# Kernel optimization log

Hardware: AMD Instinct MI355X
Metric: run time of the kernel (lower is better)

The kernel has to match this reference:

```python
import jax, jax.numpy as jnp
import numpy as np

B, S, H, V, NL = 64, 2048, 512, 50257, 2

def setup_inputs() -> dict:
    key = jax.random.key(0)
    ks = jax.random.split(key, 20)
    s = 0.02
    return {
        "input_ids": jax.random.randint(ks[0], (B,), 0, V),
        "hidden": jax.random.normal(ks[1], (NL, B, H), jnp.float32),
        "block_attn_weights": jax.random.uniform(ks[2], (B, 32), jnp.float32),
        "encoder_outputs": jax.random.normal(ks[3], (B, S, H), jnp.float32),
        "n_blocks": 32,
        "emb": jax.random.normal(ks[4], (V, H), jnp.float32) * s,
        "attn_W": jax.random.normal(ks[5], (H, H), jnp.float32) * s,
        "attn_b": jnp.zeros((H,), jnp.float32),
        "W_ih0": jax.random.normal(ks[6], (3 * H, 2 * H), jnp.float32) * s,
        "W_hh0": jax.random.normal(ks[7], (3 * H, H), jnp.float32) * s,
        "b_ih0": jnp.zeros((3 * H,), jnp.float32),
        "b_hh0": jnp.zeros((3 * H,), jnp.float32),
        "W_ih1": jax.random.normal(ks[8], (3 * H, H), jnp.float32) * s,
        "W_hh1": jax.random.normal(ks[9], (3 * H, H), jnp.float32) * s,
        "b_ih1": jnp.zeros((3 * H,), jnp.float32),
        "b_hh1": jnp.zeros((3 * H,), jnp.float32),
        "out_W": jax.random.normal(ks[10], (V, 2 * H), jnp.float32) * s,
        "out_b": jnp.zeros((V,), jnp.float32),
    }

def _gru_cell(x, h, W_ih, W_hh, b_ih, b_hh):
    gx = x @ W_ih.T + b_ih            # [B, 3H]
    gh = h @ W_hh.T + b_hh            # [B, 3H]
    xr, xz, xn = jnp.split(gx, 3, axis=-1)
    hr, hz, hn = jnp.split(gh, 3, axis=-1)
    r = jax.nn.sigmoid(xr + hr)
    z = jax.nn.sigmoid(xz + hz)
    n = jnp.tanh(xn + r * hn)
    return (1.0 - z) * n + z * h

def reference(input_ids, hidden, block_attn_weights, encoder_outputs, n_blocks,
              emb, attn_W, attn_b, W_ih0, W_hh0, b_ih0, b_hh0,
              W_ih1, W_hh1, b_ih1, b_hh1, out_W, out_b):
    b, s, h = encoder_outputs.shape
    L = s // n_blocks
    eo = encoder_outputs.reshape(b, n_blocks, L, h)          # [B,N,L,H]
    # Luong general score: h_dec . (W e + b), per block
    energy = jnp.einsum('bnlh,gh->bnlg', eo, attn_W) + attn_b  # [B,N,L,H]
    scores = jnp.einsum('bh,bnlh->bnl', hidden[-1], energy)    # [B,N,L]
    attn_w = jax.nn.softmax(scores, axis=-1)                   # [B,N,L]
    block_ctx = jnp.einsum('bnl,bnlh->bnh', attn_w, eo)        # [B,N,H]
    context = jnp.einsum('bn,bnh->bh', block_attn_weights, block_ctx)  # [B,H]
    embedded = emb[input_ids]                                  # [B,H]
    x = jnp.concatenate([embedded, context], axis=-1)          # [B,2H]
    h0 = _gru_cell(x, hidden[0], W_ih0, W_hh0, b_ih0, b_hh0)
    h1 = _gru_cell(h0, hidden[1], W_ih1, W_hh1, b_ih1, b_hh1)
    new_hidden = jnp.stack([h0, h1], axis=0)                   # [NL,B,H]
    out_in = jnp.concatenate([h1, context], axis=-1)           # [B,2H]
    log_probs = jax.nn.log_softmax(out_in @ out_W.T + out_b, axis=-1)  # [B,V]
    return (log_probs, new_hidden, context, attn_w)
```

## Files before the change

### kernel.cpp

```cpp
#include <hip/hip_runtime.h>

#define B_  64
#define S_  2048
#define H_  512
#define V_  50257
#define NB_ 32
#define L_  64
#define H3_ 1536
#define NBLK_OUT 786

typedef float  f32x4  __attribute__((ext_vector_type(4)));
typedef __bf16 bf16x8 __attribute__((ext_vector_type(8)));

struct alignas(16) U4 { unsigned int x, y, z, w; };

__device__ __forceinline__ unsigned int f2bf_bits(float f) {
  unsigned int u = __float_as_uint(f);
  return (u + 0x7fffu + ((u >> 16) & 1u)) >> 16;
}

__device__ __forceinline__ f32x4 ntload4(const float* p) {
  return __builtin_nontemporal_load((const f32x4*)p);
}

__device__ __forceinline__ bf16x8 cvt8(f32x4 w0, f32x4 w1) {
  bf16x8 r;
  r[0] = (__bf16)w0.x; r[1] = (__bf16)w0.y; r[2] = (__bf16)w0.z; r[3] = (__bf16)w0.w;
  r[4] = (__bf16)w1.x; r[5] = (__bf16)w1.y; r[6] = (__bf16)w1.z; r[7] = (__bf16)w1.w;
  return r;
}

__device__ __forceinline__ float wave_sum(float v) {
#pragma unroll
  for (int off = 32; off > 0; off >>= 1) v += __shfl_xor(v, off, 64);
  return v;
}

__global__ __launch_bounds__(128) void k_q(const float* __restrict__ hidden,
                                           const float* __restrict__ attn_W,
                                           float* __restrict__ q) {
  __shared__ float sh[2 * H_];
  int tid = threadIdx.x;
  int h  = blockIdx.x * 128 + tid;
  int b0 = blockIdx.y * 2;
  const float* h1 = hidden + B_ * H_;
  for (int i = tid; i < 2 * H_; i += 128) sh[i] = h1[b0 * H_ + i];
  __syncthreads();
  float acc0 = 0.f, acc1 = 0.f;
  for (int g = 0; g < H_; ++g) {
    float w = attn_W[(size_t)g * H_ + h];
    acc0 += sh[g] * w;
    acc1 += sh[H_ + g] * w;
  }
  q[(b0 + 0) * H_ + h] = acc0;
  q[(b0 + 1) * H_ + h] = acc1;
}

__global__ __launch_bounds__(512) void k_attn(
    const float* __restrict__ eo, const float* __restrict__ hidden,
    const float* __restrict__ attn_b, const float* __restrict__ q,
    float* __restrict__ bc, float* __restrict__ attnw_out) {
  __shared__ float sm[8], ss[8];
  __shared__ float shA[8][H_];
  int tid = threadIdx.x;
  int wv = tid >> 6, lane = tid & 63;
  int idx = blockIdx.x;
  int b = idx >> 5, n = idx & 31;

  f32x4 q0 = *(const f32x4*)(q + (size_t)b * H_ + lane * 4);
  f32x4 q1 = *(const f32x4*)(q + (size_t)b * H_ + 256 + lane * 4);

  const float* hp = hidden + (size_t)B_ * H_ + (size_t)b * H_;
  f32x4 hx = *(const f32x4*)(hp + lane * 4);
  f32x4 hy = *(const f32x4*)(hp + 256 + lane * 4);
  f32x4 ax = *(const f32x4*)(attn_b + lane * 4);
  f32x4 ay = *(const f32x4*)(attn_b + 256 + lane * 4);
  float c0 = hx.x*ax.x + hx.y*ax.y + hx.z*ax.z + hx.w*ax.w
           + hy.x*ay.x + hy.y*ay.y + hy.z*ay.z + hy.w*ay.w;
  c0 = wave_sum(c0);

  const float* eb = eo + (size_t)(b * NB_ + n) * L_ * H_ + (size_t)(wv * 8) * H_;
  float m = -1e30f, s = 0.f;
  float sall[8];
  f32x4 A0 = {0,0,0,0}, A1 = {0,0,0,0};
#pragma unroll
  for (int half = 0; half < 2; ++half) {
    const float* rb = eb + (size_t)(half * 4) * H_;
    f32x4 r0[4], r1[4];
#pragma unroll
    for (int i = 0; i < 4; ++i) {
      r0[i] = ntload4(rb + (size_t)i * H_ + lane * 4);
      r1[i] = ntload4(rb + (size_t)i * H_ + 256 + lane * 4);
    }
    float sc[4];
#pragma unroll
    for (int i = 0; i < 4; ++i)
      sc[i] = r0[i].x*q0.x + r0[i].y*q0.y + r0[i].z*q0.z + r0[i].w*q0.w
            + r1[i].x*q1.x + r1[i].y*q1.y + r1[i].z*q1.z + r1[i].w*q1.w;
#pragma unroll
    for (int off = 32; off > 0; off >>= 1) {
#pragma unroll
      for (int i = 0; i < 4; ++i) sc[i] += __shfl_xor(sc[i], off, 64);
    }
    float w[4];
#pragma unroll
    for (int i = 0; i < 4; ++i) { sc[i] += c0; sall[half * 4 + i] = sc[i]; }
    float mloc = fmaxf(fmaxf(sc[0], sc[1]), fmaxf(sc[2], sc[3]));
    float mnew = fmaxf(m, mloc);
    float alpha = __expf(m - mnew);
#pragma unroll
    for (int i = 0; i < 4; ++i) w[i] = __expf(sc[i] - mnew);
    s = s * alpha + w[0] + w[1] + w[2] + w[3];
    A0 *= alpha; A1 *= alpha;
#pragma unroll
    for (int i = 0; i < 4; ++i) {
      A0 += w[i] * r0[i];
      A1 += w[i] * r1[i];
    }
    m = mnew;
  }
  if (lane == 0) { sm[wv] = m; ss[wv] = s; }
  __syncthreads();
  float m_g = sm[0];
#pragma unroll
  for (int w = 1; w < 8; ++w) m_g = fmaxf(m_g, sm[w]);
  float s_g = 0.f;
#pragma unroll
  for (int w = 0; w < 8; ++w) s_g += ss[w] * __expf(sm[w] - m_g);
  float scale = __expf(m - m_g);
  f32x4* pa4 = (f32x4*)&shA[wv][0];
  pa4[lane]      = A0 * scale;
  pa4[64 + lane] = A1 * scale;
  __syncthreads();
  float inv = 1.f / s_g;
  float sum = 0.f;
#pragma unroll
  for (int w = 0; w < 8; ++w) sum += shA[w][tid];
  bc[(size_t)(b * NB_ + n) * H_ + tid] = sum * inv;
  if (lane == 0) {
    f32x4 e0 = {__expf(sall[0]-m_g)*inv, __expf(sall[1]-m_g)*inv,
                __expf(sall[2]-m_g)*inv, __expf(sall[3]-m_g)*inv};
    f32x4 e1 = {__expf(sall[4]-m_g)*inv, __expf(sall[5]-m_g)*inv,
                __expf(sall[6]-m_g)*inv, __expf(sall[7]-m_g)*inv};
    float* ap_ = attnw_out + (size_t)(b * NB_ + n) * L_ + wv * 8;
    *(f32x4*)ap_       = e0;
    *(f32x4*)(ap_ + 4) = e1;
  }
}

__global__ __launch_bounds__(512) void k_prep(
    const int* __restrict__ ids, const float* __restrict__ hidden,
    const float* __restrict__ baw, const float* __restrict__ emb,
    const float* __restrict__ bc, float* __restrict__ ctx,
    unsigned short* __restrict__ xcatb, unsigned short* __restrict__ h0b,
    unsigned short* __restrict__ h1b, float* __restrict__ out_ctx) {
  int b = blockIdx.x, h = threadIdx.x;
  int id = ids[b];
  float ev = emb[(size_t)id * H_ + h];
  float acc = 0.f;
  for (int n = 0; n < NB_; ++n)
    acc += baw[b * NB_ + n] * bc[(size_t)(b * NB_ + n) * H_ + h];
  ctx[b * H_ + h]      = acc;
  out_ctx[b * H_ + h]  = acc;
  xcatb[b * 1024 + h]        = (unsigned short)f2bf_bits(ev);
  xcatb[b * 1024 + 512 + h]  = (unsigned short)f2bf_bits(acc);
  h0b[b * H_ + h] = (unsigned short)f2bf_bits(hidden[b * H_ + h]);
  h1b[b * H_ + h] = (unsigned short)f2bf_bits(hidden[B_ * H_ + b * H_ + h]);
}

__global__ __launch_bounds__(256) void k_mv2(
    const float* __restrict__ W1, const float* __restrict__ bias1,
    const unsigned short* __restrict__ A1, float* __restrict__ C1, int K1,
    const float* __restrict__ W2, const float* __restrict__ bias2,
    const unsigned short* __restrict__ A2, float* __restrict__ C2, int K2) {
  bool sec = blockIdx.x >= 96;
  const float* W = sec ? W2 : W1;
  const float* bias = sec ? bias2 : bias1;
  const unsigned short* A = sec ? A2 : A1;
  float* C = sec ? C2 : C1;
  int K = sec ? K2 : K1;
  int blk = sec ? blockIdx.x - 96 : blockIdx.x;

  int tid = threadIdx.x;
  int wv = tid >> 6, lane = tid & 63;
  int mrow = lane & 15, qd = lane >> 4;
  int j = blk * 16 + mrow;
  const unsigned short* ap = A + (size_t)(wv * 16 + mrow) * K + qd * 8;
  const float* wp = W + (size_t)j * K + qd * 8;
  f32x4 acc = (f32x4){0.f, 0.f, 0.f, 0.f};
  for (int k0 = 0; k0 < K; k0 += 32) {
    bf16x8 af = __builtin_bit_cast(bf16x8, *(const U4*)(ap + k0));
    f32x4 w0 = *(const f32x4*)(wp + k0);
    f32x4 w1 = *(const f32x4*)(wp + k0 + 4);
    bf16x8 bf = cvt8(w0, w1);
    acc = __builtin_amdgcn_mfma_f32_16x16x32_bf16(af, bf, acc, 0, 0, 0);
  }
  float bv = bias[j];
#pragma unroll
  for (int r = 0; r < 4; ++r) {
    int brow = wv * 16 + qd * 4 + r;
    C[(size_t)brow * H3_ + j] = acc[r] + bv;
  }
}

__global__ __launch_bounds__(256) void k_out(
    const float* __restrict__ W, const float* __restrict__ bias,
    const unsigned short* __restrict__ A, float* __restrict__ C,
    float* __restrict__ pm, float* __restrict__ ps) {
  __shared__ float lmS[4][64], lsS[4][64];
  int tid = threadIdx.x;
  int wv = tid >> 6, lane = tid & 63;
  int mrow = lane & 15, qd = lane >> 4;
  int j = blockIdx.x * 64 + wv * 16 + mrow;
  int jc = j < V_ ? j : V_ - 1;
  const float* wp = W + (size_t)jc * 1024 + qd * 8;
  const unsigned short* ap = A + mrow * 1024 + qd * 8;
  f32x4 acc[4];
#pragma unroll
  for (int r = 0; r < 4; ++r) acc[r] = (f32x4){0.f, 0.f, 0.f, 0.f};
  for (int k0 = 0; k0 < 1024; k0 += 32) {
    f32x4 w0 = ntload4(wp + k0);
    f32x4 w1 = ntload4(wp + k0 + 4);
    bf16x8 bw = cvt8(w0, w1);
#pragma unroll
    for (int r = 0; r < 4; ++r) {
      bf16x8 af = __builtin_bit_cast(bf16x8, *(const U4*)(ap + r * 16 * 1024 + k0));
      acc[r] = __builtin_amdgcn_mfma_f32_16x16x32_bf16(af, bw, acc[r], 0, 0, 0);
    }
  }
  float bv = (j < V_) ? bias[j] : 0.f;
  if (j < V_) {
#pragma unroll
    for (int r = 0; r < 4; ++r) {
#pragma unroll
      for (int g = 0; g < 4; ++g) {
        int brow = r * 16 + qd * 4 + g;
        C[(size_t)brow * V_ + j] = acc[r][g] + bv;
      }
    }
  }
#pragma unroll
  for (int r = 0; r < 4; ++r) {
#pragma unroll
    for (int g = 0; g < 4; ++g) {
      float v = (j < V_) ? acc[r][g] + bv : -1e30f;
      float mm = v;
#pragma unroll
      for (int off = 1; off <= 8; off <<= 1)
        mm = fmaxf(mm, __shfl_xor(mm, off, 64));
      float se = __expf(v - mm);
#pragma unroll
      for (int off = 1; off <= 8; off <<= 1)
        se += __shfl_xor(se, off, 64);
      if (mrow == 0) {
        int brow = r * 16 + qd * 4 + g;
        lmS[wv][brow] = mm;
        lsS[wv][brow] = se;
      }
    }
  }
  __syncthreads();
  if (tid < 64) {
    float m = lmS[0][tid], s = lsS[0][tid];
#pragma unroll
    for (int w = 1; w < 4; ++w) {
      float mk = lmS[w][tid], sk = lsS[w][tid];
      float mn = fmaxf(m, mk);
      s = s * __expf(m - mn) + sk * __expf(mk - mn);
      m = mn;
    }
    pm[(size_t)tid * NBLK_OUT + blockIdx.x] = m;
    ps[(size_t)tid * NBLK_OUT + blockIdx.x] = s;
  }
}

__global__ __launch_bounds__(512) void k_gru(
    const float* __restrict__ gx, const float* __restrict__ gh,
    const float* __restrict__ hprev, float* __restrict__ hnew_out,
    unsigned short* __restrict__ hnew_bf, const float* __restrict__ ctx,
    unsigned short* __restrict__ outin) {
  int b = blockIdx.x, i = threadIdx.x;
  size_t g0 = (size_t)b * H3_ + i;
  float xr = gx[g0], xz = gx[g0 + 512], xn = gx[g0 + 1024];
  float hr = gh[g0], hz = gh[g0 + 512], hn = gh[g0 + 1024];
  float r  = 1.f / (1.f + __expf(-(xr + hr)));
  float z  = 1.f / (1.f + __expf(-(xz + hz)));
  float nn = tanhf(xn + r * hn);
  float hp = hprev[b * H_ + i];
  float h  = (1.f - z) * nn + z * hp;
  hnew_out[b * H_ + i] = h;
  hnew_bf[b * H_ + i]  = (unsigned short)f2bf_bits(h);
  if (outin) {
    outin[b * 1024 + i]       = (unsigned short)f2bf_bits(h);
    outin[b * 1024 + 512 + i] = (unsigned short)f2bf_bits(ctx[b * H_ + i]);
  }
}

__global__ __launch_bounds__(256) void k_wlp(const float* __restrict__ logits,
                                             const float* __restrict__ pm,
                                             const float* __restrict__ ps,
                                             float* __restrict__ out) {
  __shared__ float rm[4], rs[4];
  int tid = threadIdx.x, lane = tid & 63, wid = tid >> 6;
  int b = blockIdx.y;
  float m = -1e30f, s = 0.f;
  for (int k = tid; k < NBLK_OUT; k += 256) {
    float mk = pm[(size_t)b * NBLK_OUT + k];
    float sk = ps[(size_t)b * NBLK_OUT + k];
    float mn = fmaxf(m, mk);
    s = s * __expf(m - mn) + sk * __expf(mk - mn);
    m = mn;
  }
#pragma unroll
  for (int off = 32; off > 0; off >>= 1) {
    float mo = __shfl_xor(m, off, 64);
    float so = __shfl_xor(s, off, 64);
    float mn = fmaxf(m, mo);
    s = s * __expf(m - mn) + so * __expf(mo - mn);
    m = mn;
  }
  if (lane == 0) { rm[wid] = m; rs[wid] = s; }
  __syncthreads();
  float mg = fmaxf(fmaxf(rm[0], rm[1]), fmaxf(rm[2], rm[3]));
  float sg = rs[0] * __expf(rm[0] - mg) + rs[1] * __expf(rm[1] - mg)
           + rs[2] * __expf(rm[2] - mg) + rs[3] * __expf(rm[3] - mg);
  float lse = mg + logf(sg);
  int j = blockIdx.x * 256 + tid;
  if (j < V_) {
    float v = __builtin_nontemporal_load(logits + (size_t)b * V_ + j);
    __builtin_nontemporal_store(v - lse, out + (size_t)b * V_ + j);
  }
}

extern "C" void kernel_launch(void* const* d_in, const int* in_sizes, int n_in,
                              void* d_out, int out_size, void* d_ws, size_t ws_size,
                              hipStream_t stream) {
  const int*   ids    = (const int*)d_in[0];
  const float* hidden = (const float*)d_in[1];
  const float* baw    = (const float*)d_in[2];
  const float* eo     = (const float*)d_in[3];
  const float* emb    = (const float*)d_in[5];
  const float* attn_W = (const float*)d_in[6];
  const float* attn_b = (const float*)d_in[7];
  const float* W_ih0  = (const float*)d_in[8];
  const float* W_hh0  = (const float*)d_in[9];
  const float* b_ih0  = (const float*)d_in[10];
  const float* b_hh0  = (const float*)d_in[11];
  const float* W_ih1  = (const float*)d_in[12];
  const float* W_hh1  = (const float*)d_in[13];
  const float* b_ih1  = (const float*)d_in[14];
  const float* b_hh1  = (const float*)d_in[15];
  const float* out_W  = (const float*)d_in[16];
  const float* out_b  = (const float*)d_in[17];
  float* out = (float*)d_out;

  char* ws = (char*)d_ws;
  float*          q      = (float*)(ws + 0);
  float*          bc     = (float*)(ws + 131072);
  float*          ctx    = (float*)(ws + 4325376);
  unsigned short* xcatb  = (unsigned short*)(ws + 4456448);
  unsigned short* h0b    = (unsigned short*)(ws + 4587520);
  unsigned short* h1b    = (unsigned short*)(ws + 4653056);
  unsigned short* h0nb   = (unsigned short*)(ws + 4718592);
  unsigned short* outinb = (unsigned short*)(ws + 4784128);
  float*          gx     = (float*)(ws + 4915200);
  float*          gh     = (float*)(ws + 5308416);
  float*          logits = (float*)(ws + 5701632);
  float*          pm     = (float*)(ws + 18567424);
  float*          ps     = (float*)(ws + 18768640);

  float* out_lp   = out;
  float* out_nh   = out + 3216448;
  float* out_ctx  = out + 3281984;
  float* out_attw = out + 3314752;

  k_q   <<<dim3(4, 32), 128, 0, stream>>>(hidden, attn_W, q);
  k_attn<<<2048, 512, 0, stream>>>(eo, hidden, attn_b, q, bc, out_attw);
  k_prep<<<64, 512, 0, stream>>>(ids, hidden, baw, emb, bc, ctx, xcatb, h0b, h1b, out_ctx);

  k_mv2<<<192, 256, 0, stream>>>(W_ih0, b_ih0, xcatb, gx, 1024,
                                 W_hh0, b_hh0, h0b,   gh, 512);
  k_gru<<<64, 512, 0, stream>>>(gx, gh, hidden, out_nh, h0nb,
                                (const float*)nullptr, (unsigned short*)nullptr);

  k_mv2<<<192, 256, 0, stream>>>(W_ih1, b_ih1, h0nb, gx, 512,
                                 W_hh1, b_hh1, h1b,  gh, 512);
  k_gru<<<64, 512, 0, stream>>>(gx, gh, hidden + B_ * H_, out_nh + B_ * H_, h0nb,
                                ctx, outinb);

  k_out<<<NBLK_OUT, 256, 0, stream>>>(out_W, out_b, outinb, logits, pm, ps);
  k_wlp<<<dim3(197, 64), 256, 0, stream>>>(logits, pm, ps, out_lp);
}
```

Measured before the change: 682.8 us.

## Fuse prep, GRU matvecs and cells into one persistent kernel with grid barriers

Replaces five separate launches (prep, two mv2, two gru) with one 192-block kernel that separates phases with an atomic-counter grid barrier; the counter is reset in k_q. This removes launch gaps and tail idle time between small dependent kernels. The attention loop also now processes two rows at a time instead of batches of four, which reduces register pressure but gives less memory-level parallelism per wave. The grid barrier relies on all 192 blocks being co-resident, and its correctness depends on that.

New measurement: 735.4 us. +7.7%, slower.

```diff
diff --git a/kernel.cpp b/kernel.cpp
--- a/kernel.cpp
+++ b/kernel.cpp
@@ -8,6 +8,7 @@
 #define L_  64
 #define H3_ 1536
 #define NBLK_OUT 786
+#define FUSE_BLKS 192
 
 typedef float  f32x4  __attribute__((ext_vector_type(4)));
 typedef __bf16 bf16x8 __attribute__((ext_vector_type(8)));
@@ -36,9 +37,24 @@
   return v;
 }
 
+__device__ __forceinline__ void gridbar(int* cnt, int target) {
+  __syncthreads();
+  if (threadIdx.x == 0) {
+    __threadfence();
+    __hip_atomic_fetch_add(cnt, 1, __ATOMIC_RELAXED, __HIP_MEMORY_SCOPE_AGENT);
+    while (__hip_atomic_load(cnt, __ATOMIC_RELAXED, __HIP_MEMORY_SCOPE_AGENT) < target)
+      __builtin_amdgcn_s_sleep(2);
+    __threadfence();
+  }
+  __syncthreads();
+}
+
 __global__ __launch_bounds__(128) void k_q(const float* __restrict__ hidden,
                                            const float* __restrict__ attn_W,
-                                           float* __restrict__ q) {
+                                           float* __restrict__ q,
+                                           int* __restrict__ cnt) {
+  if (blockIdx.x == 0 && blockIdx.y == 0 && threadIdx.x == 0)
+    __hip_atomic_store(cnt, 0, __ATOMIC_RELAXED, __HIP_MEMORY_SCOPE_AGENT);
   __shared__ float sh[2 * H_];
   int tid = threadIdx.x;
   int h  = blockIdx.x * 128 + tid;
@@ -84,39 +100,31 @@
   float sall[8];
   f32x4 A0 = {0,0,0,0}, A1 = {0,0,0,0};
 #pragma unroll
-  for (int half = 0; half < 2; ++half) {
-    const float* rb = eb + (size_t)(half * 4) * H_;
-    f32x4 r0[4], r1[4];
-#pragma unroll
-    for (int i = 0; i < 4; ++i) {
-      r0[i] = ntload4(rb + (size_t)i * H_ + lane * 4);
-      r1[i] = ntload4(rb + (size_t)i * H_ + 256 + lane * 4);
-    }
-    float sc[4];
-#pragma unroll
-    for (int i = 0; i < 4; ++i)
-      sc[i] = r0[i].x*q0.x + r0[i].y*q0.y + r0[i].z*q0.z + r0[i].w*q0.w
-            + r1[i].x*q1.x + r1[i].y*q1.y + r1[i].z*q1.z + r1[i].w*q1.w;
+  for (int lr = 0; lr < 8; lr += 2) {
+    const float* rA = eb + (size_t)lr * H_;
+    const float* rB = rA + H_;
+    f32x4 a0 = ntload4(rA + lane * 4);
+    f32x4 a1 = ntload4(rA + 256 + lane * 4);
+    f32x4 b0 = ntload4(rB + lane * 4);
+    f32x4 b1 = ntload4(rB + 256 + lane * 4);
+    float pa = a0.x*q0.x + a0.y*q0.y + a0.z*q0.z + a0.w*q0.w
+             + a1.x*q1.x + a1.y*q1.y + a1.z*q1.z + a1.w*q1.w;
+    float pb = b0.x*q0.x + b0.y*q0.y + b0.z*q0.z + b0.w*q0.w
+             + b1.x*q1.x + b1.y*q1.y + b1.z*q1.z + b1.w*q1.w;
 #pragma unroll
     for (int off = 32; off > 0; off >>= 1) {
-#pragma unroll
-      for (int i = 0; i < 4; ++i) sc[i] += __shfl_xor(sc[i], off, 64);
-    }
-    float w[4];
-#pragma unroll
-    for (int i = 0; i < 4; ++i) { sc[i] += c0; sall[half * 4 + i] = sc[i]; }
-    float mloc = fmaxf(fmaxf(sc[0], sc[1]), fmaxf(sc[2], sc[3]));
-    float mnew = fmaxf(m, mloc);
+      pa += __shfl_xor(pa, off, 64);
+      pb += __shfl_xor(pb, off, 64);
+    }
+    pa += c0; pb += c0;
+    sall[lr] = pa; sall[lr + 1] = pb;
+    float mnew  = fmaxf(m, fmaxf(pa, pb));
     float alpha = __expf(m - mnew);
-#pragma unroll
-    for (int i = 0; i < 4; ++i) w[i] = __expf(sc[i] - mnew);
-    s = s * alpha + w[0] + w[1] + w[2] + w[3];
-    A0 *= alpha; A1 *= alpha;
-#pragma unroll
-    for (int i = 0; i < 4; ++i) {
-      A0 += w[i] * r0[i];
-      A1 += w[i] * r1[i];
-    }
+    float wa    = __expf(pa - mnew);
+    float wb    = __expf(pb - mnew);
+    s = s * alpha + wa + wb;
+    A0 = A0 * alpha + wa * a0 + wb * b0;
+    A1 = A1 * alpha + wa * a1 + wb * b1;
     m = mnew;
   }
   if (lane == 0) { sm[wv] = m; ss[wv] = s; }
@@ -148,27 +156,7 @@
   }
 }
 
-__global__ __launch_bounds__(512) void k_prep(
-    const int* __restrict__ ids, const float* __restrict__ hidden,
-    const float* __restrict__ baw, const float* __restrict__ emb,
-    const float* __restrict__ bc, float* __restrict__ ctx,
-    unsigned short* __restrict__ xcatb, unsigned short* __restrict__ h0b,
-    unsigned short* __restrict__ h1b, float* __restrict__ out_ctx) {
-  int b = blockIdx.x, h = threadIdx.x;
-  int id = ids[b];
-  float ev = emb[(size_t)id * H_ + h];
-  float acc = 0.f;
-  for (int n = 0; n < NB_; ++n)
-    acc += baw[b * NB_ + n] * bc[(size_t)(b * NB_ + n) * H_ + h];
-  ctx[b * H_ + h]      = acc;
-  out_ctx[b * H_ + h]  = acc;
-  xcatb[b * 1024 + h]        = (unsigned short)f2bf_bits(ev);
-  xcatb[b * 1024 + 512 + h]  = (unsigned short)f2bf_bits(acc);
-  h0b[b * H_ + h] = (unsigned short)f2bf_bits(hidden[b * H_ + h]);
-  h1b[b * H_ + h] = (unsigned short)f2bf_bits(hidden[B_ * H_ + b * H_ + h]);
-}
-
-__global__ __launch_bounds__(256) void k_mv2(
+__device__ __forceinline__ void mv2_phase(
     const float* __restrict__ W1, const float* __restrict__ bias1,
     const unsigned short* __restrict__ A1, float* __restrict__ C1, int K1,
     const float* __restrict__ W2, const float* __restrict__ bias2,
@@ -203,6 +191,73 @@
   }
 }
 
+__device__ __forceinline__ void gru_phase(
+    const float* __restrict__ gx, const float* __restrict__ gh,
+    const float* __restrict__ hprev, float* __restrict__ hnew_out,
+    unsigned short* __restrict__ hnew_bf, const float* __restrict__ ctx,
+    unsigned short* __restrict__ outin) {
+  int item = blockIdx.x * 256 + threadIdx.x;
+  if (item < B_ * H_) {
+    int b = item >> 9, i = item & 511;
+    size_t g0 = (size_t)b * H3_ + i;
+    float xr = gx[g0], xz = gx[g0 + 512], xn = gx[g0 + 1024];
+    float hr = gh[g0], hz = gh[g0 + 512], hn = gh[g0 + 1024];
+    float r  = 1.f / (1.f + __expf(-(xr + hr)));
+    float z  = 1.f / (1.f + __expf(-(xz + hz)));
+    float nn = tanhf(xn + r * hn);
+    float hp = hprev[b * H_ + i];
+    float h  = (1.f - z) * nn + z * hp;
+    hnew_out[b * H_ + i] = h;
+    if (hnew_bf) hnew_bf[b * H_ + i] = (unsigned short)f2bf_bits(h);
+    if (outin) {
+      outin[b * 1024 + i]       = (unsigned short)f2bf_bits(h);
+      outin[b * 1024 + 512 + i] = (unsigned short)f2bf_bits(ctx[b * H_ + i]);
+    }
+  }
+}
+
+__global__ __launch_bounds__(256) void k_fuse(
+    const int* __restrict__ ids, const float* __restrict__ hidden,
+    const float* __restrict__ baw, const float* __restrict__ emb,
+    const float* __restrict__ bc, float* __restrict__ ctx,
+    unsigned short* __restrict__ xcatb, unsigned short* __restrict__ h0b,
+    unsigned short* __restrict__ h1b, float* __restrict__ out_ctx,
+    const float* __restrict__ W_ih0, const float* __restrict__ b_ih0,
+    const float* __restrict__ W_hh0, const float* __restrict__ b_hh0,
+    const float* __restrict__ W_ih1, const float* __restrict__ b_ih1,
+    const float* __restrict__ W_hh1, const float* __restrict__ b_hh1,
+    float* __restrict__ gx, float* __restrict__ gh,
+    float* __restrict__ out_nh, unsigned short* __restrict__ h0nb,
+    unsigned short* __restrict__ outinb, int* __restrict__ cnt) {
+  {
+    int item = blockIdx.x * 256 + threadIdx.x;
+    if (item < B_ * H_) {
+      int b = item >> 9, h = item & 511;
+      int id = ids[b];
+      float ev = emb[(size_t)id * H_ + h];
+      float acc = 0.f;
+      for (int n = 0; n < NB_; ++n)
+        acc += baw[b * NB_ + n] * bc[(size_t)(b * NB_ + n) * H_ + h];
+      ctx[b * H_ + h]      = acc;
+      out_ctx[b * H_ + h]  = acc;
+      xcatb[b * 1024 + h]        = (unsigned short)f2bf_bits(ev);
+      xcatb[b * 1024 + 512 + h]  = (unsigned short)f2bf_bits(acc);
+      h0b[b * H_ + h] = (unsigned short)f2bf_bits(hidden[b * H_ + h]);
+      h1b[b * H_ + h] = (unsigned short)f2bf_bits(hidden[B_ * H_ + b * H_ + h]);
+    }
+  }
+  gridbar(cnt, 1 * FUSE_BLKS);
+  mv2_phase(W_ih0, b_ih0, xcatb, gx, 1024, W_hh0, b_hh0, h0b, gh, 512);
+  gridbar(cnt, 2 * FUSE_BLKS);
+  gru_phase(gx, gh, hidden, out_nh, h0nb, (const float*)nullptr,
+            (unsigned short*)nullptr);
+  gridbar(cnt, 3 * FUSE_BLKS);
+  mv2_phase(W_ih1, b_ih1, h0nb, gx, 512, W_hh1, b_hh1, h1b, gh, 512);
+  gridbar(cnt, 4 * FUSE_BLKS);
+  gru_phase(gx, gh, hidden + B_ * H_, out_nh + B_ * H_,
+            (unsigned short*)nullptr, ctx, outinb);
+}
+
 __global__ __launch_bounds__(256) void k_out(
     const float* __restrict__ W, const float* __restrict__ bias,
     const unsigned short* __restrict__ A, float* __restrict__ C,
@@ -271,28 +326,6 @@
     }
     pm[(size_t)tid * NBLK_OUT + blockIdx.x] = m;
     ps[(size_t)tid * NBLK_OUT + blockIdx.x] = s;
-  }
-}
-
-__global__ __launch_bounds__(512) void k_gru(
-    const float* __restrict__ gx, const float* __restrict__ gh,
-    const float* __restrict__ hprev, float* __restrict__ hnew_out,
-    unsigned short* __restrict__ hnew_bf, const float* __restrict__ ctx,
-    unsigned short* __restrict__ outin) {
-  int b = blockIdx.x, i = threadIdx.x;
-  size_t g0 = (size_t)b * H3_ + i;
-  float xr = gx[g0], xz = gx[g0 + 512], xn = gx[g0 + 1024];
-  float hr = gh[g0], hz = gh[g0 + 512], hn = gh[g0 + 1024];
-  float r  = 1.f / (1.f + __expf(-(xr + hr)));
-  float z  = 1.f / (1.f + __expf(-(xz + hz)));
-  float nn = tanhf(xn + r * hn);
-  float hp = hprev[b * H_ + i];
-  float h  = (1.f - z) * nn + z * hp;
-  hnew_out[b * H_ + i] = h;
-  hnew_bf[b * H_ + i]  = (unsigned short)f2bf_bits(h);
-  if (outin) {
-    outin[b * 1024 + i]       = (unsigned short)f2bf_bits(h);
-    outin[b * 1024 + 512 + i] = (unsigned short)f2bf_bits(ctx[b * H_ + i]);
   }
 }
 
@@ -368,26 +401,20 @@
   float*          logits = (float*)(ws + 5701632);
   float*          pm     = (float*)(ws + 18567424);
   float*          ps     = (float*)(ws + 18768640);
+  int*            cnt    = (int*)  (ws + 18969856);
 
   float* out_lp   = out;
   float* out_nh   = out + 3216448;
   float* out_ctx  = out + 3281984;
   float* out_attw = out + 3314752;
 
-  k_q   <<<dim3(4, 32), 128, 0, stream>>>(hidden, attn_W, q);
+  k_q   <<<dim3(4, 32), 128, 0, stream>>>(hidden, attn_W, q, cnt);
   k_attn<<<2048, 512, 0, stream>>>(eo, hidden, attn_b, q, bc, out_attw);
-  k_prep<<<64, 512, 0, stream>>>(ids, hidden, baw, emb, bc, ctx, xcatb, h0b, h1b, out_ctx);
-
-  k_mv2<<<192, 256, 0, stream>>>(W_ih0, b_ih0, xcatb, gx, 1024,
-                                 W_hh0, b_hh0, h0b,   gh, 512);
-  k_gru<<<64, 512, 0, stream>>>(gx, gh, hidden, out_nh, h0nb,
-                                (const float*)nullptr, (unsigned short*)nullptr);
-
-  k_mv2<<<192, 256, 0, stream>>>(W_ih1, b_ih1, h0nb, gx, 512,
-                                 W_hh1, b_hh1, h1b,  gh, 512);
-  k_gru<<<64, 512, 0, stream>>>(gx, gh, hidden + B_ * H_, out_nh + B_ * H_, h0nb,
-                                ctx, outinb);
-
+  k_fuse<<<FUSE_BLKS, 256, 0, stream>>>(ids, hidden, baw, emb, bc, ctx,
+                                        xcatb, h0b, h1b, out_ctx,
+                                        W_ih0, b_ih0, W_hh0, b_hh0,
+                                        W_ih1, b_ih1, W_hh1, b_hh1,
+                                        gx, gh, out_nh, h0nb, outinb, cnt);
   k_out<<<NBLK_OUT, 256, 0, stream>>>(out_W, out_b, outinb, logits, pm, ps);
   k_wlp<<<dim3(197, 64), 256, 0, stream>>>(logits, pm, ps, out_lp);
 }
```
